# Kernel tuning notes

Measured on AMD Instinct MI355X. Metric: run time of the kernel, lower is better.

## Reference

```python
import jax, jax.numpy as jnp
import numpy as np

EMBED_DIM = 1024
NUM_HEADS = 16
HEAD_DIM = EMBED_DIM // NUM_HEADS
B, S = 4, 2048


def setup_inputs() -> dict:
    key = jax.random.key(0)
    ks = jax.random.split(key, 9)
    sc = 1.0 / np.sqrt(EMBED_DIM)
    d = {"x": jax.random.normal(ks[0], (B, S, EMBED_DIM), jnp.float32)}
    for i, name in enumerate(["q", "k", "v", "out"]):
        d[f"w_{name}"] = jax.random.uniform(ks[1 + 2 * i], (EMBED_DIM, EMBED_DIM), jnp.float32, -sc, sc)
        d[f"b_{name}"] = jax.random.uniform(ks[2 + 2 * i], (EMBED_DIM,), jnp.float32, -sc, sc)
    return d


def reference(x, w_q, b_q, w_k, b_k, w_v, b_v, w_out, b_out):
    b, s, e = x.shape
    # projections (PyTorch Linear: x @ W.T + b)
    q = (x @ w_q.T + b_q).reshape(b, s, NUM_HEADS, HEAD_DIM).transpose(0, 2, 1, 3)
    k = (x @ w_k.T + b_k).reshape(b, s, NUM_HEADS, HEAD_DIM).transpose(0, 2, 1, 3)
    v = (x @ w_v.T + b_v).reshape(b, s, NUM_HEADS, HEAD_DIM).transpose(0, 2, 1, 3)
    scores = jnp.einsum("bhqd,bhkd->bhqk", q, k) / np.sqrt(HEAD_DIM).astype(np.float32)
    attn = jax.nn.softmax(scores, axis=-1)  # dropout p=0.0 -> identity
    out = jnp.einsum("bhqk,bhkd->bhqd", attn, v)
    out = out.transpose(0, 2, 1, 3).reshape(b, s, e)
    return out @ w_out.T + b_out
```

## Files before the change

### kernel.cpp

```cpp
#include <hip/hip_runtime.h>


typedef __bf16 bf16x8 __attribute__((ext_vector_type(8)));
typedef float  f32x4  __attribute__((ext_vector_type(4)));
typedef unsigned short u16x4 __attribute__((ext_vector_type(4)));

#define BB 4
#define SS 2048
#define EE 1024
#define HH 16
#define DD 64
#define MM 8192
#define GK 1024
#define GN 1024

static __device__ __forceinline__ unsigned short f2bf(float f) {
  unsigned int u = __float_as_uint(f);
  u += 0x7fffu + ((u >> 16) & 1u);
  return (unsigned short)(u >> 16);
}

static __device__ __forceinline__ void gld_lds16(const void* g, void* l) {
  __builtin_amdgcn_global_load_lds((__attribute__((address_space(1))) void*)g,
                                   (__attribute__((address_space(3))) void*)l,
                                   16, 0, 0);
}

__global__ __launch_bounds__(256) void cvt_all(
    const float* __restrict__ x,  const float* __restrict__ wq,
    const float* __restrict__ wk, const float* __restrict__ wv,
    const float* __restrict__ wo,
    unsigned short* __restrict__ xb,  unsigned short* __restrict__ wqb,
    unsigned short* __restrict__ wkb, unsigned short* __restrict__ wvb,
    unsigned short* __restrict__ wob) {
  const unsigned long long NX = 8ull * 1024 * 1024;
  const unsigned long long NW = 1024ull * 1024;
  unsigned long long i = (unsigned long long)blockIdx.x * 256 + threadIdx.x;
  unsigned long long e = i * 4;
  const float* src; unsigned short* dst; unsigned long long off;
  if (e < NX) { src = x; dst = xb; off = e; }
  else {
    unsigned long long j = e - NX;
    unsigned int wi = (unsigned int)(j >> 20);
    off = j & (NW - 1);
    src = (wi == 0) ? wq : (wi == 1) ? wk : (wi == 2) ? wv : wo;
    dst = (wi == 0) ? wqb : (wi == 1) ? wkb : (wi == 2) ? wvb : wob;
  }
  float4 v = *(const float4*)(src + off);
  u16x4 o; o.x = f2bf(v.x); o.y = f2bf(v.y); o.z = f2bf(v.z); o.w = f2bf(v.w);
  *(u16x4*)(dst + off) = o;
}

template <int MODE>
__global__ __launch_bounds__(256, 2) void gemm_bt(
    const unsigned short* __restrict__ A, const unsigned short* __restrict__ Bt,
    const float* __restrict__ bias, void* __restrict__ Cout, float oscale) {
  __shared__ __align__(16) unsigned short As[128 * 64];
  __shared__ __align__(16) unsigned short Bs[128 * 64];
  const int tid = threadIdx.x, lane = tid & 63, w = tid >> 6;
  const int l15 = lane & 15, quad = lane >> 4;
  const int wm = w & 1, wn = w >> 1;
  const int m0 = blockIdx.y * 128, n0 = blockIdx.x * 128;

  f32x4 acc[4][4] = {};

  for (int k0 = 0; k0 < GK; k0 += 64) {
    __syncthreads();
#pragma unroll
    for (int t = 0; t < 4; ++t) {
      int cb = (w * 4 + t) * 64;
      int c = cb + lane, r = c >> 3, g = ((c & 7) + r) & 7;
      gld_lds16(A + (size_t)(m0 + r) * GK + k0 + g * 8, &As[cb * 8]);
    }
#pragma unroll
    for (int t = 0; t < 4; ++t) {
      int cb = (w * 4 + t) * 64;
      int c = cb + lane, r = c >> 3, g = ((c & 7) + r) & 7;
      gld_lds16(Bt + (size_t)(n0 + r) * GK + k0 + g * 8, &Bs[cb * 8]);
    }
    __builtin_amdgcn_s_waitcnt(0);
    __syncthreads();
#pragma unroll
    for (int ks = 0; ks < 2; ++ks) {
      const int s = (ks * 4 + quad - l15) & 7;
      bf16x8 af[4], bfr[4];
#pragma unroll
      for (int mi = 0; mi < 4; ++mi)
        af[mi] = *(const bf16x8*)&As[(wm * 64 + mi * 16 + l15) * 64 + s * 8];
#pragma unroll
      for (int ni = 0; ni < 4; ++ni)
        bfr[ni] = *(const bf16x8*)&Bs[(wn * 64 + ni * 16 + l15) * 64 + s * 8];
#pragma unroll
      for (int mi = 0; mi < 4; ++mi)
#pragma unroll
        for (int ni = 0; ni < 4; ++ni)
          acc[mi][ni] = __builtin_amdgcn_mfma_f32_16x16x32_bf16(
              af[mi], bfr[ni], acc[mi][ni], 0, 0, 0);
    }
  }
#pragma unroll
  for (int ni = 0; ni < 4; ++ni) {
    int n = n0 + wn * 64 + ni * 16 + l15;
    float bv = bias[n];
#pragma unroll
    for (int mi = 0; mi < 4; ++mi) {
#pragma unroll
      for (int r = 0; r < 4; ++r) {
        int m = m0 + wm * 64 + mi * 16 + quad * 4 + r;
        float cv = (acc[mi][ni][r] + bv) * oscale;
        if (MODE == 0) {
          int b = m >> 11, s = m & 2047, h = n >> 6, d = n & 63;
          ((unsigned short*)Cout)[(((size_t)(b * HH + h) * SS + s) * DD) + d] = f2bf(cv);
        } else if (MODE == 1) {
          int b = m >> 11, s = m & 2047, h = n >> 6, d = n & 63;
          ((unsigned short*)Cout)[(((size_t)(b * HH + h) * DD + d) * SS) + s] = f2bf(cv);
        } else {
          ((float*)Cout)[(size_t)m * GN + n] = cv;
        }
      }
    }
  }
}

__global__ __launch_bounds__(256, 3) void attn(
    const unsigned short* __restrict__ Q,
    const unsigned short* __restrict__ K,
    const unsigned short* __restrict__ Vt,
    unsigned short* __restrict__ O) {
  __shared__ __align__(16) unsigned short Ks[2][64 * 64];
  __shared__ __align__(16) unsigned short Vs[2][64 * 64];
  __shared__ __align__(16) unsigned short Ps[4 * 16 * 72];
  const int tid = threadIdx.x, lane = tid & 63, w = tid >> 6;
  const int l15 = lane & 15, quad = lane >> 4;
  const int bh = blockIdx.x >> 5;
  const int q0 = (blockIdx.x & 31) * 64;
  const int b = bh >> 4, h = bh & 15;

  const unsigned short* Qb = Q + (size_t)bh * SS * DD;
  const unsigned short* Kb = K + (size_t)bh * SS * DD;
  const unsigned short* Vb = Vt + (size_t)bh * DD * SS;

  const int qrow = q0 + w * 16 + l15;
  bf16x8 qf0 = *(const bf16x8*)&Qb[(size_t)qrow * DD + quad * 8];
  bf16x8 qf1 = *(const bf16x8*)&Qb[(size_t)qrow * DD + 32 + quad * 8];

  f32x4 oacc[4] = {};
  float lrow[4] = {0.f, 0.f, 0.f, 0.f};
  unsigned short* Pw = &Ps[w * 16 * 72];

#pragma unroll
  for (int t = 0; t < 2; ++t) {
    int cb = (w * 2 + t) * 64;
    int c = cb + lane, r = c >> 3, g = ((c & 7) + r) & 7;
    gld_lds16(Kb + (size_t)r * DD + g * 8, &Ks[0][cb * 8]);
    gld_lds16(Vb + (size_t)r * SS + g * 8, &Vs[0][cb * 8]);
  }
  __syncthreads();

  for (int kt = 0; kt < SS / 64; ++kt) {
    const int cur = kt & 1;
    if (kt + 1 < SS / 64) {
      const int k0n = (kt + 1) * 64, nxt = cur ^ 1;
#pragma unroll
      for (int t = 0; t < 2; ++t) {
        int cb = (w * 2 + t) * 64;
        int c = cb + lane, r = c >> 3, g = ((c & 7) + r) & 7;
        gld_lds16(Kb + (size_t)(k0n + r) * DD + g * 8, &Ks[nxt][cb * 8]);
        gld_lds16(Vb + (size_t)r * SS + k0n + g * 8, &Vs[nxt][cb * 8]);
      }
    }
    const unsigned short* Kc = Ks[cur];
    const unsigned short* Vc = Vs[cur];
#pragma unroll
    for (int nt = 0; nt < 4; ++nt) {
      f32x4 z = {};
#pragma unroll
      for (int ks = 0; ks < 2; ++ks) {
        const int s = (ks * 4 + quad - l15) & 7;
        const bf16x8 kf = *(const bf16x8*)&Kc[(nt * 16 + l15) * 64 + s * 8];
        z = __builtin_amdgcn_mfma_f32_16x16x32_bf16(ks ? qf1 : qf0, kf, z, 0, 0, 0);
      }
#pragma unroll
      for (int r = 0; r < 4; ++r) {
        float p = __expf(z[r]);
        lrow[r] += p;
        Pw[(quad * 4 + r) * 72 + nt * 16 + l15] = f2bf(p);
      }
    }
    bf16x8 pf0 = *(const bf16x8*)&Pw[l15 * 72 + quad * 8];
    bf16x8 pf1 = *(const bf16x8*)&Pw[l15 * 72 + 32 + quad * 8];
#pragma unroll
    for (int nt = 0; nt < 4; ++nt) {
#pragma unroll
      for (int kc = 0; kc < 2; ++kc) {
        const int s = (kc * 4 + quad - l15) & 7;
        const bf16x8 vf = *(const bf16x8*)&Vc[(nt * 16 + l15) * 64 + s * 8];
        oacc[nt] = __builtin_amdgcn_mfma_f32_16x16x32_bf16(
            kc ? pf1 : pf0, vf, oacc[nt], 0, 0, 0);
      }
    }
    __syncthreads();
  }
#pragma unroll
  for (int r = 0; r < 4; ++r) {
    float t = lrow[r];
    t += __shfl_xor(t, 1);
    t += __shfl_xor(t, 2);
    t += __shfl_xor(t, 4);
    t += __shfl_xor(t, 8);
    float inv = 1.0f / t;
    int qr = q0 + w * 16 + quad * 4 + r;
#pragma unroll
    for (int nt = 0; nt < 4; ++nt)
      O[((size_t)b * SS + qr) * EE + h * 64 + nt * 16 + l15] = f2bf(oacc[nt][r] * inv);
  }
}

extern "C" void kernel_launch(void* const* d_in, const int* in_sizes, int n_in,
                              void* d_out, int out_size, void* d_ws, size_t ws_size,
                              hipStream_t stream) {
  const float* x  = (const float*)d_in[0];
  const float* wq = (const float*)d_in[1];
  const float* bq = (const float*)d_in[2];
  const float* wk = (const float*)d_in[3];
  const float* bk = (const float*)d_in[4];
  const float* wv = (const float*)d_in[5];
  const float* bv = (const float*)d_in[6];
  const float* wo = (const float*)d_in[7];
  const float* bo = (const float*)d_in[8];

  unsigned short* ws = (unsigned short*)d_ws;
  const size_t MEG = 1024ull * 1024;
  unsigned short* xb  = ws;
  unsigned short* wqb = ws + 8 * MEG;
  unsigned short* wkb = ws + 9 * MEG;
  unsigned short* wvb = ws + 10 * MEG;
  unsigned short* wob = ws + 11 * MEG;
  unsigned short* qb  = ws + 12 * MEG;
  unsigned short* kb  = ws + 20 * MEG;
  unsigned short* vtb = ws + 28 * MEG;
  unsigned short* ob  = xb;

  cvt_all<<<12288, 256, 0, stream>>>(x, wq, wk, wv, wo, xb, wqb, wkb, wvb, wob);
  dim3 gg(GN / 128, MM / 128);
  gemm_bt<0><<<gg, 256, 0, stream>>>(xb, wqb, bq, qb, 0.125f);
  gemm_bt<0><<<gg, 256, 0, stream>>>(xb, wkb, bk, kb, 1.0f);
  gemm_bt<1><<<gg, 256, 0, stream>>>(xb, wvb, bv, vtb, 1.0f);
  attn<<<BB * HH * (SS / 64), 256, 0, stream>>>(qb, kb, vtb, ob);
  gemm_bt<2><<<gg, 256, 0, stream>>>(ob, wob, bo, d_out, 1.0f);
}
```

Baseline: 328.0 us.

## Fuse Q/K projections, vectorize GEMM epilogues, register-only P in attention

```diff
diff --git a/kernel.cpp b/kernel.cpp
--- a/kernel.cpp
+++ b/kernel.cpp
@@ -2,6 +2,8 @@
 
 
 typedef __bf16 bf16x8 __attribute__((ext_vector_type(8)));
+typedef __bf16 bf16x2 __attribute__((ext_vector_type(2)));
+typedef __bf16 bf16x4v __attribute__((ext_vector_type(4)));
 typedef float  f32x4  __attribute__((ext_vector_type(4)));
 typedef unsigned short u16x4 __attribute__((ext_vector_type(4)));
 
@@ -52,15 +54,28 @@
 }
 
 template <int MODE>
-__global__ __launch_bounds__(256, 2) void gemm_bt(
-    const unsigned short* __restrict__ A, const unsigned short* __restrict__ Bt,
-    const float* __restrict__ bias, void* __restrict__ Cout, float oscale) {
+__global__ __launch_bounds__(256, 2) void gemm2(
+    const unsigned short* __restrict__ A,
+    const unsigned short* __restrict__ B0, const unsigned short* __restrict__ B1,
+    const float* __restrict__ bias0, const float* __restrict__ bias1,
+    void* __restrict__ out0, void* __restrict__ out1) {
   __shared__ __align__(16) unsigned short As[128 * 64];
   __shared__ __align__(16) unsigned short Bs[128 * 64];
   const int tid = threadIdx.x, lane = tid & 63, w = tid >> 6;
   const int l15 = lane & 15, quad = lane >> 4;
   const int wm = w & 1, wn = w >> 1;
-  const int m0 = blockIdx.y * 128, n0 = blockIdx.x * 128;
+  const int m0 = blockIdx.y * 128;
+
+  const unsigned short* Bt; const float* bias; void* out; float osc; int n0w;
+  if (MODE == 0) {
+    int sel = (blockIdx.x >= 8);
+    Bt = sel ? B1 : B0; bias = sel ? bias1 : bias0; out = sel ? out1 : out0;
+    osc = sel ? 1.0f : 0.125f;
+    n0w = (blockIdx.x & 7) * 128;
+  } else {
+    Bt = B0; bias = bias0; out = out0; osc = 1.0f;
+    n0w = blockIdx.x * 128;
+  }
 
   f32x4 acc[4][4] = {};
 
@@ -76,7 +91,7 @@
     for (int t = 0; t < 4; ++t) {
       int cb = (w * 4 + t) * 64;
       int c = cb + lane, r = c >> 3, g = ((c & 7) + r) & 7;
-      gld_lds16(Bt + (size_t)(n0 + r) * GK + k0 + g * 8, &Bs[cb * 8]);
+      gld_lds16(Bt + (size_t)(n0w + r) * GK + k0 + g * 8, &Bs[cb * 8]);
     }
     __builtin_amdgcn_s_waitcnt(0);
     __syncthreads();
@@ -93,29 +108,53 @@
 #pragma unroll
       for (int mi = 0; mi < 4; ++mi)
 #pragma unroll
-        for (int ni = 0; ni < 4; ++ni)
-          acc[mi][ni] = __builtin_amdgcn_mfma_f32_16x16x32_bf16(
-              af[mi], bfr[ni], acc[mi][ni], 0, 0, 0);
-    }
-  }
-#pragma unroll
-  for (int ni = 0; ni < 4; ++ni) {
-    int n = n0 + wn * 64 + ni * 16 + l15;
-    float bv = bias[n];
-#pragma unroll
-    for (int mi = 0; mi < 4; ++mi) {
-#pragma unroll
-      for (int r = 0; r < 4; ++r) {
-        int m = m0 + wm * 64 + mi * 16 + quad * 4 + r;
-        float cv = (acc[mi][ni][r] + bv) * oscale;
+        for (int ni = 0; ni < 4; ++ni) {
+          if (MODE == 1)
+            acc[mi][ni] = __builtin_amdgcn_mfma_f32_16x16x32_bf16(
+                af[mi], bfr[ni], acc[mi][ni], 0, 0, 0);
+          else
+            acc[ni][mi] = __builtin_amdgcn_mfma_f32_16x16x32_bf16(
+                bfr[ni], af[mi], acc[ni][mi], 0, 0, 0);
+        }
+    }
+  }
+  if (MODE == 1) {
+#pragma unroll
+    for (int ni = 0; ni < 4; ++ni) {
+      int n = n0w + wn * 64 + ni * 16 + l15;
+      float bv = bias[n];
+      int h = n >> 6, d = n & 63;
+#pragma unroll
+      for (int mi = 0; mi < 4; ++mi) {
+        int mb = m0 + wm * 64 + mi * 16 + quad * 4;
+        int b = mb >> 11, s = mb & 2047;
+        bf16x4v o;
+#pragma unroll
+        for (int r = 0; r < 4; ++r) o[r] = (__bf16)(acc[mi][ni][r] + bv);
+        *(bf16x4v*)&((unsigned short*)out)[((size_t)(b * HH + h) * DD + d) * SS + s] = o;
+      }
+    }
+  } else {
+#pragma unroll
+    for (int ni = 0; ni < 4; ++ni) {
+      int nb = n0w + wn * 64 + ni * 16 + quad * 4;
+      float4 b4 = *(const float4*)&bias[nb];
+#pragma unroll
+      for (int mi = 0; mi < 4; ++mi) {
+        int m = m0 + wm * 64 + mi * 16 + l15;
         if (MODE == 0) {
-          int b = m >> 11, s = m & 2047, h = n >> 6, d = n & 63;
-          ((unsigned short*)Cout)[(((size_t)(b * HH + h) * SS + s) * DD) + d] = f2bf(cv);
-        } else if (MODE == 1) {
-          int b = m >> 11, s = m & 2047, h = n >> 6, d = n & 63;
-          ((unsigned short*)Cout)[(((size_t)(b * HH + h) * DD + d) * SS) + s] = f2bf(cv);
+          int b = m >> 11, s = m & 2047, h = nb >> 6, d = nb & 63;
+          bf16x4v o;
+          o[0] = (__bf16)((acc[ni][mi][0] + b4.x) * osc);
+          o[1] = (__bf16)((acc[ni][mi][1] + b4.y) * osc);
+          o[2] = (__bf16)((acc[ni][mi][2] + b4.z) * osc);
+          o[3] = (__bf16)((acc[ni][mi][3] + b4.w) * osc);
+          *(bf16x4v*)&((unsigned short*)out)[((size_t)(b * HH + h) * SS + s) * DD + d] = o;
         } else {
-          ((float*)Cout)[(size_t)m * GN + n] = cv;
+          float4 st;
+          st.x = acc[ni][mi][0] + b4.x; st.y = acc[ni][mi][1] + b4.y;
+          st.z = acc[ni][mi][2] + b4.z; st.w = acc[ni][mi][3] + b4.w;
+          *(float4*)&((float*)out)[(size_t)m * GN + nb] = st;
         }
       }
     }
@@ -129,24 +168,29 @@
     unsigned short* __restrict__ O) {
   __shared__ __align__(16) unsigned short Ks[2][64 * 64];
   __shared__ __align__(16) unsigned short Vs[2][64 * 64];
-  __shared__ __align__(16) unsigned short Ps[4 * 16 * 72];
   const int tid = threadIdx.x, lane = tid & 63, w = tid >> 6;
   const int l15 = lane & 15, quad = lane >> 4;
-  const int bh = blockIdx.x >> 5;
-  const int q0 = (blockIdx.x & 31) * 64;
+  const int bh = blockIdx.x >> 4;
+  const int q0 = (blockIdx.x & 15) * 128;
   const int b = bh >> 4, h = bh & 15;
 
   const unsigned short* Qb = Q + (size_t)bh * SS * DD;
   const unsigned short* Kb = K + (size_t)bh * SS * DD;
   const unsigned short* Vb = Vt + (size_t)bh * DD * SS;
 
-  const int qrow = q0 + w * 16 + l15;
-  bf16x8 qf0 = *(const bf16x8*)&Qb[(size_t)qrow * DD + quad * 8];
-  bf16x8 qf1 = *(const bf16x8*)&Qb[(size_t)qrow * DD + 32 + quad * 8];
-
-  f32x4 oacc[4] = {};
-  float lrow[4] = {0.f, 0.f, 0.f, 0.f};
-  unsigned short* Pw = &Ps[w * 16 * 72];
+  bf16x8 qf[2][2];
+#pragma unroll
+  for (int qb = 0; qb < 2; ++qb) {
+    int qrow = q0 + w * 32 + qb * 16 + l15;
+    qf[qb][0] = *(const bf16x8*)&Qb[(size_t)qrow * DD + quad * 8];
+    qf[qb][1] = *(const bf16x8*)&Qb[(size_t)qrow * DD + 32 + quad * 8];
+  }
+
+  f32x4 oaccT[4][2] = {};
+  float lrow[2] = {0.f, 0.f};
+  const int qodd = quad & 1;
+  const int Rcore = (l15 >> 2) * 8 + (l15 & 3);
+  const int Rpar = ((l15 >> 2) & 1) * 4;
 
 #pragma unroll
   for (int t = 0; t < 2; ++t) {
@@ -171,48 +215,69 @@
     }
     const unsigned short* Kc = Ks[cur];
     const unsigned short* Vc = Vs[cur];
-#pragma unroll
-    for (int nt = 0; nt < 4; ++nt) {
-      f32x4 z = {};
+
+    int pk[2][2][2][2];
+#pragma unroll
+    for (int ks = 0; ks < 2; ++ks)
+#pragma unroll
+      for (int beta = 0; beta < 2; ++beta) {
+        const int R = ks * 32 + Rcore + (beta ? (4 - Rpar) : Rpar);
+        const int s0 = (quad - R) & 7, s1 = (4 + quad - R) & 7;
+        const bf16x8 kf0 = *(const bf16x8*)&Kc[R * 64 + s0 * 8];
+        const bf16x8 kf1 = *(const bf16x8*)&Kc[R * 64 + s1 * 8];
+#pragma unroll
+        for (int qb = 0; qb < 2; ++qb) {
+          f32x4 z = {};
+          z = __builtin_amdgcn_mfma_f32_16x16x32_bf16(kf0, qf[qb][0], z, 0, 0, 0);
+          z = __builtin_amdgcn_mfma_f32_16x16x32_bf16(kf1, qf[qb][1], z, 0, 0, 0);
+          float p0 = __expf(z[0]), p1 = __expf(z[1]);
+          float p2 = __expf(z[2]), p3 = __expf(z[3]);
+          lrow[qb] += (p0 + p1) + (p2 + p3);
+          union { bf16x2 h2; int i; } ua, ub;
+          ua.h2.x = (__bf16)p0; ua.h2.y = (__bf16)p1;
+          ub.h2.x = (__bf16)p2; ub.h2.y = (__bf16)p3;
+          pk[qb][ks][beta][0] = ua.i; pk[qb][ks][beta][1] = ub.i;
+        }
+      }
+    union PB { int i[4]; bf16x8 v; } pf[2][2];
+#pragma unroll
+    for (int qb = 0; qb < 2; ++qb)
 #pragma unroll
       for (int ks = 0; ks < 2; ++ks) {
-        const int s = (ks * 4 + quad - l15) & 7;
-        const bf16x8 kf = *(const bf16x8*)&Kc[(nt * 16 + l15) * 64 + s * 8];
-        z = __builtin_amdgcn_mfma_f32_16x16x32_bf16(ks ? qf1 : qf0, kf, z, 0, 0, 0);
-      }
-#pragma unroll
-      for (int r = 0; r < 4; ++r) {
-        float p = __expf(z[r]);
-        lrow[r] += p;
-        Pw[(quad * 4 + r) * 72 + nt * 16 + l15] = f2bf(p);
-      }
-    }
-    bf16x8 pf0 = *(const bf16x8*)&Pw[l15 * 72 + quad * 8];
-    bf16x8 pf1 = *(const bf16x8*)&Pw[l15 * 72 + 32 + quad * 8];
-#pragma unroll
-    for (int nt = 0; nt < 4; ++nt) {
-#pragma unroll
-      for (int kc = 0; kc < 2; ++kc) {
-        const int s = (kc * 4 + quad - l15) & 7;
-        const bf16x8 vf = *(const bf16x8*)&Vc[(nt * 16 + l15) * 64 + s * 8];
-        oacc[nt] = __builtin_amdgcn_mfma_f32_16x16x32_bf16(
-            kc ? pf1 : pf0, vf, oacc[nt], 0, 0, 0);
+        pf[qb][ks].i[0] = qodd ? pk[qb][ks][1][0] : pk[qb][ks][0][0];
+        pf[qb][ks].i[1] = qodd ? pk[qb][ks][1][1] : pk[qb][ks][0][1];
+        pf[qb][ks].i[2] = qodd ? pk[qb][ks][0][0] : pk[qb][ks][1][0];
+        pf[qb][ks].i[3] = qodd ? pk[qb][ks][0][1] : pk[qb][ks][1][1];
+      }
+#pragma unroll
+    for (int mb = 0; mb < 4; ++mb) {
+      const int s0 = (quad - l15) & 7, s1 = (4 + quad - l15) & 7;
+      const bf16x8 vf0 = *(const bf16x8*)&Vc[(mb * 16 + l15) * 64 + s0 * 8];
+      const bf16x8 vf1 = *(const bf16x8*)&Vc[(mb * 16 + l15) * 64 + s1 * 8];
+#pragma unroll
+      for (int qb = 0; qb < 2; ++qb) {
+        oaccT[mb][qb] = __builtin_amdgcn_mfma_f32_16x16x32_bf16(
+            vf0, pf[qb][0].v, oaccT[mb][qb], 0, 0, 0);
+        oaccT[mb][qb] = __builtin_amdgcn_mfma_f32_16x16x32_bf16(
+            vf1, pf[qb][1].v, oaccT[mb][qb], 0, 0, 0);
       }
     }
     __syncthreads();
   }
 #pragma unroll
-  for (int r = 0; r < 4; ++r) {
-    float t = lrow[r];
-    t += __shfl_xor(t, 1);
-    t += __shfl_xor(t, 2);
-    t += __shfl_xor(t, 4);
-    t += __shfl_xor(t, 8);
-    float inv = 1.0f / t;
-    int qr = q0 + w * 16 + quad * 4 + r;
-#pragma unroll
-    for (int nt = 0; nt < 4; ++nt)
-      O[((size_t)b * SS + qr) * EE + h * 64 + nt * 16 + l15] = f2bf(oacc[nt][r] * inv);
+  for (int qb = 0; qb < 2; ++qb) {
+    float l = lrow[qb];
+    l += __shfl_xor(l, 16);
+    l += __shfl_xor(l, 32);
+    float inv = 1.0f / l;
+    int q = q0 + w * 32 + qb * 16 + l15;
+#pragma unroll
+    for (int mb = 0; mb < 4; ++mb) {
+      bf16x4v o;
+#pragma unroll
+      for (int r = 0; r < 4; ++r) o[r] = (__bf16)(oaccT[mb][qb][r] * inv);
+      *(bf16x4v*)&O[((size_t)b * SS + q) * EE + h * 64 + mb * 16 + quad * 4] = o;
+    }
   }
 }
 
@@ -242,10 +307,8 @@
   unsigned short* ob  = xb;
 
   cvt_all<<<12288, 256, 0, stream>>>(x, wq, wk, wv, wo, xb, wqb, wkb, wvb, wob);
-  dim3 gg(GN / 128, MM / 128);
-  gemm_bt<0><<<gg, 256, 0, stream>>>(xb, wqb, bq, qb, 0.125f);
-  gemm_bt<0><<<gg, 256, 0, stream>>>(xb, wkb, bk, kb, 1.0f);
-  gemm_bt<1><<<gg, 256, 0, stream>>>(xb, wvb, bv, vtb, 1.0f);
-  attn<<<BB * HH * (SS / 64), 256, 0, stream>>>(qb, kb, vtb, ob);
-  gemm_bt<2><<<gg, 256, 0, stream>>>(ob, wob, bo, d_out, 1.0f);
-}
+  gemm2<0><<<dim3(16, 64), 256, 0, stream>>>(xb, wqb, wkb, bq, bk, qb, kb);
+  gemm2<1><<<dim3(8, 64), 256, 0, stream>>>(xb, wvb, nullptr, bv, nullptr, vtb, nullptr);
+  attn<<<BB * HH * (SS / 128), 256, 0, stream>>>(qb, kb, vtb, ob);
+  gemm2<2><<<dim3(8, 64), 256, 0, stream>>>(ob, wob, nullptr, bo, nullptr, d_out, nullptr);
+}
```

New measurement: 282.5 us. 13.9% less time.
